# Optimization experiments

Measured on AMD Instinct MI355X. Metric: run time of the kernel, lower is better.

Reference implementation:

```python
import jax, jax.numpy as jnp
import numpy as np

STD = 2.5  # fixed Gaussian std in the original module
K = 5      # hard-coded pdf support: range(5)


def _gauss_weights(segment_len, max_chunk):
    """Vectorized replacement of the scipy per-chunk loop.

    segment_len: [B] int (num_chunks per batch element)
    returns weights: [B, max_chunk, K] float32
    """
    n = segment_len.astype(jnp.float32)                      # [B]
    i = jnp.arange(max_chunk, dtype=jnp.float32)             # [M]
    x = jnp.arange(K, dtype=jnp.float32)                     # [K]
    denom = jnp.where(n > 1.0, n - 1.0, 1.0)                 # avoid div-by-zero for n==1
    mu = i[None, :] * 4.0 / denom[:, None]                   # [B, M]
    # Gaussian pdf up to a constant factor; constant cancels in min-max norm.
    z = (x[None, None, :] - mu[:, :, None]) / STD            # [B, M, K]
    l = jnp.exp(-0.5 * z * z)                                # [B, M, K]
    lmin = l.min(axis=-1, keepdims=True)
    lmax = l.max(axis=-1, keepdims=True)
    w = (l - lmin) / (lmax - lmin)                           # min-max normalize per row
    # zero out rows i >= num_chunks (frame initialized to zeros)
    valid = (jnp.arange(max_chunk)[None, :] < segment_len[:, None])[:, :, None]
    w = jnp.where(valid, w, 0.0)
    # special case num_chunks == 1: frame[:1] = 1.0 (entire first row ones)
    one_case = jnp.where(jnp.arange(max_chunk)[None, :, None] == 0, 1.0, 0.0)
    w = jnp.where((segment_len == 1)[:, None, None], one_case, w)
    return w.astype(jnp.float32)


def setup_inputs() -> dict:
    key = jax.random.key(0)
    k1, k2 = jax.random.split(key)
    B, D, M = 64, 1024, 512
    segment_len = jax.random.randint(k1, (B,), 1, M + 1).astype(jnp.int64)
    Q_emb = jax.random.normal(k2, (B, K, D), dtype=jnp.float32)
    return {"segment_len": segment_len, "max_chunk": M, "Q_emb": Q_emb}


def reference(segment_len, max_chunk, Q_emb):
    w = _gauss_weights(segment_len, max_chunk)               # [B, M, K]
    return jnp.einsum('bmk,bkd->bmd', w, Q_emb)              # [B, M, D]
```

## Files before the change

### kernel.cpp

```cpp
#include <hip/hip_runtime.h>


#define K_SUP 5

__global__ __launch_bounds__(256)
void gauss_xattn_kernel(const int* __restrict__ seg,
                        const float* __restrict__ Q,
                        float* __restrict__ out,
                        int M, int D) {
    const int bm = blockIdx.x;
    const int m = bm % M;
    const int b = bm / M;
    const int n = seg[b];

    float w[K_SUP];
    bool zero_row;
    if (n == 1) {
        zero_row = (m != 0);
        #pragma unroll
        for (int k = 0; k < K_SUP; ++k) w[k] = 1.0f;
    } else if (m >= n) {
        zero_row = true;
        #pragma unroll
        for (int k = 0; k < K_SUP; ++k) w[k] = 0.0f;
    } else {
        zero_row = false;
        const float mu = (float)m * 4.0f / (float)(n - 1);
        float l[K_SUP];
        #pragma unroll
        for (int k = 0; k < K_SUP; ++k) {
            const float z = ((float)k - mu) * (1.0f / 2.5f);
            l[k] = __expf(-0.5f * z * z);
        }
        const float lmin = fminf(fminf(fminf(l[0], l[1]), fminf(l[2], l[3])), l[4]);
        const float lmax = fmaxf(fmaxf(fmaxf(l[0], l[1]), fmaxf(l[2], l[3])), l[4]);
        const float inv = 1.0f / (lmax - lmin);
        #pragma unroll
        for (int k = 0; k < K_SUP; ++k) w[k] = (l[k] - lmin) * inv;
    }

    const float* __restrict__ Qb = Q + (size_t)b * K_SUP * D;
    float* __restrict__ orow = out + (size_t)bm * D;

    for (int d = threadIdx.x * 4; d < D; d += blockDim.x * 4) {
        float4 o;
        if (zero_row) {
            o = make_float4(0.0f, 0.0f, 0.0f, 0.0f);
        } else {
            float4 acc = make_float4(0.0f, 0.0f, 0.0f, 0.0f);
            #pragma unroll
            for (int k = 0; k < K_SUP; ++k) {
                const float4 q = *reinterpret_cast<const float4*>(Qb + (size_t)k * D + d);
                acc.x += w[k] * q.x;
                acc.y += w[k] * q.y;
                acc.z += w[k] * q.z;
                acc.w += w[k] * q.w;
            }
            o = acc;
        }
        *reinterpret_cast<float4*>(orow + d) = o;
    }
}

extern "C" void kernel_launch(void* const* d_in, const int* in_sizes, int n_in,
                              void* d_out, int out_size, void* d_ws, size_t ws_size,
                              hipStream_t stream) {
    const int*   seg = (const int*)d_in[0];
    const float* Q   = (const float*)d_in[2];
    float*       out = (float*)d_out;

    const int B = in_sizes[0];
    const int D = in_sizes[2] / (B * K_SUP);
    const int M = out_size / (B * D);

    dim3 grid(B * M);
    gauss_xattn_kernel<<<grid, 256, 0, stream>>>(seg, Q, out, M, D);
}
```

Measured before the change: 29.82 us.

## Process 16 output rows per block reusing Q registers with nontemporal stores

Each block now handles 16 consecutive m rows instead of one, loading the five Q vectors once into registers and reusing them across rows. Q loads are skipped when the whole group is past the valid length, and outputs are written with nontemporal stores. This cuts the grid size and repeated Q reads, at the cost of assuming D equals 1024 (256 threads times 4) and M divisible by 16.

```diff
diff --git a/kernel.cpp b/kernel.cpp
--- a/kernel.cpp
+++ b/kernel.cpp
@@ -2,63 +2,62 @@
 
 
 #define K_SUP 5
+#define ROWS  16
+
+typedef float f32x4 __attribute__((ext_vector_type(4)));
 
 __global__ __launch_bounds__(256)
 void gauss_xattn_kernel(const int* __restrict__ seg,
                         const float* __restrict__ Q,
                         float* __restrict__ out,
                         int M, int D) {
-    const int bm = blockIdx.x;
-    const int m = bm % M;
-    const int b = bm / M;
-    const int n = seg[b];
+    const int groups_per_b = M / ROWS;
+    const int g  = blockIdx.x;
+    const int b  = g / groups_per_b;
+    const int m0 = (g % groups_per_b) * ROWS;
+    const int n  = seg[b];
+    const int d  = threadIdx.x * 4;
 
-    float w[K_SUP];
-    bool zero_row;
-    if (n == 1) {
-        zero_row = (m != 0);
+    f32x4 q[K_SUP];
+    const bool need_q = (m0 < n) || (n == 1 && m0 == 0);
+    if (need_q) {
+        const float* __restrict__ Qb = Q + ((size_t)b * K_SUP) * D + d;
         #pragma unroll
-        for (int k = 0; k < K_SUP; ++k) w[k] = 1.0f;
-    } else if (m >= n) {
-        zero_row = true;
-        #pragma unroll
-        for (int k = 0; k < K_SUP; ++k) w[k] = 0.0f;
-    } else {
-        zero_row = false;
-        const float mu = (float)m * 4.0f / (float)(n - 1);
-        float l[K_SUP];
-        #pragma unroll
-        for (int k = 0; k < K_SUP; ++k) {
-            const float z = ((float)k - mu) * (1.0f / 2.5f);
-            l[k] = __expf(-0.5f * z * z);
-        }
-        const float lmin = fminf(fminf(fminf(l[0], l[1]), fminf(l[2], l[3])), l[4]);
-        const float lmax = fmaxf(fmaxf(fmaxf(l[0], l[1]), fmaxf(l[2], l[3])), l[4]);
-        const float inv = 1.0f / (lmax - lmin);
-        #pragma unroll
-        for (int k = 0; k < K_SUP; ++k) w[k] = (l[k] - lmin) * inv;
+        for (int k = 0; k < K_SUP; ++k)
+            q[k] = *reinterpret_cast<const f32x4*>(Qb + (size_t)k * D);
     }
 
-    const float* __restrict__ Qb = Q + (size_t)b * K_SUP * D;
-    float* __restrict__ orow = out + (size_t)bm * D;
+    float* __restrict__ orow = out + ((size_t)(b * M + m0)) * D + d;
 
-    for (int d = threadIdx.x * 4; d < D; d += blockDim.x * 4) {
-        float4 o;
-        if (zero_row) {
-            o = make_float4(0.0f, 0.0f, 0.0f, 0.0f);
-        } else {
-            float4 acc = make_float4(0.0f, 0.0f, 0.0f, 0.0f);
+    #pragma unroll
+    for (int r = 0; r < ROWS; ++r, orow += D) {
+        const int m = m0 + r;
+        f32x4 o = (f32x4)(0.0f);
+
+        if (n == 1) {
+            if (m == 0) {
+                #pragma unroll
+                for (int k = 0; k < K_SUP; ++k) o += q[k];
+            }
+        } else if (m < n) {
+            const float mu = (float)m * 4.0f / (float)(n - 1);
+            float l[K_SUP];
             #pragma unroll
             for (int k = 0; k < K_SUP; ++k) {
-                const float4 q = *reinterpret_cast<const float4*>(Qb + (size_t)k * D + d);
-                acc.x += w[k] * q.x;
-                acc.y += w[k] * q.y;
-                acc.z += w[k] * q.z;
-                acc.w += w[k] * q.w;
+                const float z = ((float)k - mu) * (1.0f / 2.5f);
+                l[k] = __expf(-0.5f * z * z);
             }
-            o = acc;
+            const float lmin = fminf(fminf(fminf(l[0], l[1]), fminf(l[2], l[3])), l[4]);
+            const float lmax = fmaxf(fmaxf(fmaxf(l[0], l[1]), fmaxf(l[2], l[3])), l[4]);
+            const float inv = 1.0f / (lmax - lmin);
+            #pragma unroll
+            for (int k = 0; k < K_SUP; ++k) {
+                const float wk = (l[k] - lmin) * inv;
+                o += wk * q[k];
+            }
         }
-        *reinterpret_cast<float4*>(orow + d) = o;
+
+        __builtin_nontemporal_store(o, reinterpret_cast<f32x4*>(orow));
     }
 }
 
@@ -73,6 +72,6 @@
     const int D = in_sizes[2] / (B * K_SUP);
     const int M = out_size / (B * D);
 
-    dim3 grid(B * M);
+    dim3 grid(B * (M / ROWS));
     gauss_xattn_kernel<<<grid, 256, 0, stream>>>(seg, Q, out, M, D);
 }
```

After: 34.41 us. +15.4%, slower.
